# Performance work log

Hardware: AMD Instinct MI355X
Metric: run time of the kernel (lower is better)

The kernel has to match this reference:

```python
import jax, jax.numpy as jnp
import numpy as np

EPS = 1e-5

def layer_norm(x, gamma, beta):
    m = jnp.mean(x, axis=-1, keepdims=True)
    v = jnp.var(x, axis=-1, keepdims=True)
    return (x - m) / jnp.sqrt(v + EPS) * gamma + beta


def setup_inputs() -> dict:
    key = jax.random.key(0)
    ks = jax.random.split(key, 10)
    B, N, D = 2, 2048, 1024
    H, Dh = 16, 64
    C, CD = 256, 512
    inner = H * Dh  # 1024
    J = C + 1 + N  # 2305 = context + null + self

    x = jax.random.normal(ks[0], (B, N, D), dtype=jnp.float32)
    context = jax.random.normal(ks[1], (B, C, CD), dtype=jnp.float32)
    mask = jax.random.uniform(ks[2], (B, C + N)) < 0.9  # bool, mostly True
    attn_bias = jax.random.normal(ks[3], (H, N, J), dtype=jnp.float32) * 0.02

    norm_gamma = jnp.ones((D,), dtype=jnp.float32)
    null_kv = jax.random.normal(ks[4], (2, Dh), dtype=jnp.float32)
    Wq = jax.random.normal(ks[5], (D, inner), dtype=jnp.float32) * (D ** -0.5)
    Wkv = jax.random.normal(ks[6], (D, 2 * Dh), dtype=jnp.float32) * (D ** -0.5)
    ctx_ln_w = jnp.ones((CD,), dtype=jnp.float32)
    ctx_ln_b = jnp.zeros((CD,), dtype=jnp.float32)
    Wctx = jax.random.normal(ks[7], (CD, 2 * Dh), dtype=jnp.float32) * (CD ** -0.5)
    bctx = jnp.zeros((2 * Dh,), dtype=jnp.float32)
    Wout = jax.random.normal(ks[8], (inner, D), dtype=jnp.float32) * (inner ** -0.5)
    out_gamma = jnp.ones((D,), dtype=jnp.float32)

    return {"x": x, "context": context, "mask": mask, "attn_bias": attn_bias,
            "norm_gamma": norm_gamma, "null_kv": null_kv, "Wq": Wq, "Wkv": Wkv,
            "ctx_ln_w": ctx_ln_w, "ctx_ln_b": ctx_ln_b, "Wctx": Wctx, "bctx": bctx,
            "Wout": Wout, "out_gamma": out_gamma}


def reference(x, context, mask, attn_bias, norm_gamma, null_kv, Wq, Wkv,
              ctx_ln_w, ctx_ln_b, Wctx, bctx, Wout, out_gamma):
    B, N, D = x.shape
    Dh = null_kv.shape[-1]
    H = Wq.shape[-1] // Dh
    scale = Dh ** -0.5

    xn = layer_norm(x, norm_gamma, 0.0)
    q = (xn @ Wq).reshape(B, N, H, Dh).transpose(0, 2, 1, 3) * scale  # b h n d
    k, v = jnp.split(xn @ Wkv, 2, axis=-1)  # b n d each (multi-query: shared across heads)

    # prepend learned null kv token
    nk = jnp.broadcast_to(null_kv[0], (B, 1, Dh))
    nv = jnp.broadcast_to(null_kv[1], (B, 1, Dh))
    k = jnp.concatenate([nk, k], axis=1)
    v = jnp.concatenate([nv, v], axis=1)

    # prepend projected context tokens
    cn = layer_norm(context, ctx_ln_w, ctx_ln_b)
    ck, cv = jnp.split(cn @ Wctx + bctx, 2, axis=-1)
    k = jnp.concatenate([ck, k], axis=1)  # b j d, j = C + 1 + N
    v = jnp.concatenate([cv, v], axis=1)

    sim = jnp.einsum('bhid,bjd->bhij', q, k) + attn_bias
    # pad mask with True for the null token (left), then broadcast over h, i
    m = jnp.pad(mask, ((0, 0), (1, 0)), constant_values=True)[:, None, None, :]
    max_neg = -jnp.finfo(sim.dtype).max
    sim = jnp.where(m, sim, max_neg)

    attn = jax.nn.softmax(sim.astype(jnp.float32), axis=-1)
    out = jnp.einsum('bhij,bjd->bhid', attn, v)  # b h n d
    out = out.transpose(0, 2, 1, 3).reshape(B, N, H * Dh)
    return layer_norm(out @ Wout, out_gamma, 0.0)
```

## Files before the change

### kernel.cpp

```cpp
#include <hip/hip_runtime.h>

constexpr int B  = 2;
constexpr int N  = 2048;
constexpr int H  = 16;
constexpr int C  = 256;
constexpr int J  = C + 1 + N;
constexpr int Jp = 2368;
constexpr int NT = Jp / 64;
constexpr float EPS = 1e-5f;
constexpr float LOG2E = 1.4426950408889634f;

typedef __bf16 bf16x8 __attribute__((ext_vector_type(8)));
typedef float  f32x4  __attribute__((ext_vector_type(4)));
typedef unsigned int uint4v __attribute__((ext_vector_type(4)));
typedef __attribute__((address_space(3))) unsigned int lds_u32;
typedef const __attribute__((address_space(1))) unsigned int glb_u32;

__device__ inline void load_lds16(const void* g, void* l) {
    __builtin_amdgcn_global_load_lds((glb_u32*)g, (lds_u32*)l, 16, 0, 0);
}
__device__ inline unsigned short f2bf(float f) {
    unsigned int u = __builtin_bit_cast(unsigned int, f);
    u += 0x7fffu + ((u >> 16) & 1u);
    return (unsigned short)(u >> 16);
}
__device__ inline unsigned int packbf2(float a, float b) {
    union { __bf16 h[2]; unsigned int u; } cv;
    cv.h[0] = (__bf16)a;
    cv.h[1] = (__bf16)b;
    return cv.u;
}
__device__ inline float fexp2(float x) {
    float r;
    asm("v_exp_f32 %0, %1" : "=v"(r) : "v"(x));
    return r;
}
__device__ inline f32x4 mfma16(bf16x8 a, bf16x8 b, f32x4 c) {
    return __builtin_amdgcn_mfma_f32_16x16x32_bf16(a, b, c, 0, 0, 0);
}
__device__ inline f32x4 loadu4(const float* p) {
    f32x4 r;
    __builtin_memcpy(&r, p, 16);
    return r;
}

__global__ void mask_prep(const void* __restrict__ mraw, float* __restrict__ maskf) {
    __shared__ int bad_int, bad_f32;
    const int t = threadIdx.x;
    if (t == 0) { bad_int = 0; bad_f32 = 0; }
    __syncthreads();
    const unsigned int* w = (const unsigned int*)mraw;
    int li = 0, lf = 0;
    for (int i = t; i < 1152; i += 256) {
        unsigned int v = w[i];
        if (v > 1u) li = 1;
        if (v != 0u && v != 0x3F800000u) lf = 1;
    }
    if (li) atomicOr(&bad_int, 1);
    if (lf) atomicOr(&bad_f32, 1);
    __syncthreads();
    const int mode = (!bad_int) ? 0 : ((!bad_f32) ? 1 : 2);
    const unsigned char* bytes = (const unsigned char*)mraw;
    for (int i = t; i < 2 * Jp; i += 256) {
        const int b2 = i / Jp, jp = i - b2 * Jp;
        float v;
        if (jp == 0) v = 0.f;
        else if (jp >= J) v = -1e30f;
        else {
            const int idx = b2 * (C + N) + jp - 1;
            const int keep = (mode == 2) ? (bytes[idx] != 0) : (w[idx] != 0u);
            v = keep ? 0.f : -1e30f;
        }
        maskf[i] = v;
    }
}

__global__ void zero_pads(unsigned short* __restrict__ Kb, unsigned short* __restrict__ Vt) {
    const int t = threadIdx.x;
    for (int i = t; i < 2 * 63 * 64; i += 256) {
        const int b2 = i / (63 * 64);
        const int rr = (i / 64) % 63;
        const int d  = i % 64;
        Kb[(size_t)(b2 * Jp + J + rr) * 64 + d] = 0;
    }
    for (int i = t; i < 2 * 64 * 63; i += 256) {
        const int b2 = i / (64 * 63);
        const int d  = (i / 63) % 64;
        const int cc = i % 63;
        Vt[(size_t)(b2 * 64 + d) * Jp + J + cc] = 0;
    }
}

template <int BF16OUT>
__global__ void __launch_bounds__(256) ln1024(const float* __restrict__ x,
                                              const float* __restrict__ gamma,
                                              void* __restrict__ outp) {
    const int row = blockIdx.x;
    const int t = threadIdx.x;
    const float* xr = x + (size_t)row * 1024;
    float4 v = ((const float4*)xr)[t];
    float s  = v.x + v.y + v.z + v.w;
    float ss = v.x * v.x + v.y * v.y + v.z * v.z + v.w * v.w;
    #pragma unroll
    for (int o = 1; o < 64; o <<= 1) {
        s  += __shfl_xor(s, o);
        ss += __shfl_xor(ss, o);
    }
    __shared__ float red[8];
    const int w = t >> 6;
    if ((t & 63) == 0) { red[w * 2] = s; red[w * 2 + 1] = ss; }
    __syncthreads();
    s  = red[0] + red[2] + red[4] + red[6];
    ss = red[1] + red[3] + red[5] + red[7];
    const float mean = s * (1.0f / 1024.0f);
    const float var  = ss * (1.0f / 1024.0f) - mean * mean;
    const float rstd = rsqrtf(var + EPS);
    const float4 g = ((const float4*)gamma)[t];
    float o0 = (v.x - mean) * rstd * g.x;
    float o1 = (v.y - mean) * rstd * g.y;
    float o2 = (v.z - mean) * rstd * g.z;
    float o3 = (v.w - mean) * rstd * g.w;
    if (BF16OUT) {
        ushort4 u;
        u.x = f2bf(o0); u.y = f2bf(o1); u.z = f2bf(o2); u.w = f2bf(o3);
        *(ushort4*)((unsigned short*)outp + (size_t)row * 1024 + t * 4) = u;
    } else {
        *(float4*)((float*)outp + (size_t)row * 1024 + t * 4) = make_float4(o0, o1, o2, o3);
    }
}

__global__ void __launch_bounds__(256) transpose_w(const float* __restrict__ W,
                                                   unsigned short* __restrict__ WT,
                                                   int K, int Nn, float scale) {
    __shared__ float lds[64][68];
    const int k0 = blockIdx.x * 64, n0 = blockIdx.y * 64;
    const int t = threadIdx.x;
    const int kk = t >> 4, nn = (t & 15) * 4;
    #pragma unroll
    for (int r = 0; r < 4; r++) {
        const float4 v = *(const float4*)(W + (size_t)(k0 + kk + r * 16) * Nn + n0 + nn);
        lds[kk + r * 16][nn + 0] = v.x;
        lds[kk + r * 16][nn + 1] = v.y;
        lds[kk + r * 16][nn + 2] = v.z;
        lds[kk + r * 16][nn + 3] = v.w;
    }
    __syncthreads();
    const int nr = t >> 2, kc = (t & 3) * 16;
    #pragma unroll
    for (int u4 = 0; u4 < 4; u4++) {
        ushort4 u;
        u.x = f2bf(lds[kc + u4 * 4 + 0][nr] * scale);
        u.y = f2bf(lds[kc + u4 * 4 + 1][nr] * scale);
        u.z = f2bf(lds[kc + u4 * 4 + 2][nr] * scale);
        u.w = f2bf(lds[kc + u4 * 4 + 3][nr] * scale);
        *(ushort4*)(WT + (size_t)(n0 + nr) * K + k0 + kc + u4 * 4) = u;
    }
}

__global__ void __launch_bounds__(128) ctx_proj(const float* __restrict__ ctx,
                                                const float* __restrict__ lw,
                                                const float* __restrict__ lb,
                                                const float* __restrict__ Wc,
                                                const float* __restrict__ bc,
                                                unsigned short* __restrict__ Kb,
                                                unsigned short* __restrict__ Vt) {
    const int row = blockIdx.x;
    const int b2 = row >> 8, ci = row & 255;
    const int t = threadIdx.x;
    __shared__ float cn[512];
    __shared__ float red[4];
    const float* xr = ctx + (size_t)row * 512;
    float4 v = ((const float4*)xr)[t];
    float s  = v.x + v.y + v.z + v.w;
    float ss = v.x * v.x + v.y * v.y + v.z * v.z + v.w * v.w;
    #pragma unroll
    for (int o = 1; o < 64; o <<= 1) {
        s  += __shfl_xor(s, o);
        ss += __shfl_xor(ss, o);
    }
    const int w = t >> 6;
    if ((t & 63) == 0) { red[w * 2] = s; red[w * 2 + 1] = ss; }
    __syncthreads();
    s  = red[0] + red[2];
    ss = red[1] + red[3];
    const float mean = s * (1.0f / 512.0f);
    const float var  = ss * (1.0f / 512.0f) - mean * mean;
    const float rstd = rsqrtf(var + EPS);
    const float4 g  = ((const float4*)lw)[t];
    const float4 be = ((const float4*)lb)[t];
    float4 c4;
    c4.x = (v.x - mean) * rstd * g.x + be.x;
    c4.y = (v.y - mean) * rstd * g.y + be.y;
    c4.z = (v.z - mean) * rstd * g.z + be.z;
    c4.w = (v.w - mean) * rstd * g.w + be.w;
    *(float4*)&cn[t * 4] = c4;
    __syncthreads();
    float acc = bc[t];
    #pragma unroll 8
    for (int d = 0; d < 512; d++) acc = fmaf(cn[d], Wc[d * 128 + t], acc);
    const unsigned short bv = f2bf(acc);
    if (t < 64) Kb[(size_t)(b2 * Jp + ci) * 64 + t] = bv;
    else        Vt[(size_t)(b2 * 64 + (t - 64)) * Jp + ci] = bv;
}

__global__ void null_fill(const float* __restrict__ nkv,
                          unsigned short* __restrict__ Kb, unsigned short* __restrict__ Vt) {
    const int b2 = blockIdx.x;
    const int t = threadIdx.x;
    Kb[(size_t)(b2 * Jp + 256) * 64 + t] = f2bf(nkv[t]);
    Vt[(size_t)(b2 * 64 + t) * Jp + 256] = f2bf(nkv[64 + t]);
}

template <int MODE>
__global__ void __launch_bounds__(256, 2) gemm_bf16(
        const unsigned short* __restrict__ A, const unsigned short* __restrict__ BT,
        float* __restrict__ Cf, unsigned short* __restrict__ Cb,
        unsigned short* __restrict__ Kb, unsigned short* __restrict__ Vt,
        int M, int Nn, int K) {
    __shared__ __align__(16) unsigned char smem[65536];
    const int t = threadIdx.x;
    const int w = t >> 6, lane = t & 63;
    const int g = lane >> 4, ln15 = lane & 15;
    const int wm = w >> 1, wn = w & 1;
    const int row0 = blockIdx.x * 128, col0 = blockIdx.y * 128;
    const int nk = K >> 6;
    const int ls = lane >> 3;
    const int swz = (lane & 7) ^ ls;

    f32x4 acc[4][4];
    #pragma unroll
    for (int i = 0; i < 4; i++)
        #pragma unroll
        for (int jj = 0; jj < 4; jj++)
            acc[i][jj] = (f32x4){0.f, 0.f, 0.f, 0.f};

    auto stage = [&](int kt, int cur) {
        if (w < 2) {
            const unsigned short* src = A + (size_t)(row0 + w * 64 + ls) * K + kt * 64 + swz * 8;
            unsigned char* dst = smem + cur * 16384 + w * 8192;
            #pragma unroll
            for (int i = 0; i < 8; i++)
                load_lds16(src + (size_t)i * 8 * K, dst + i * 1024);
        } else {
            const unsigned short* src = BT + (size_t)(col0 + (w - 2) * 64 + ls) * K + kt * 64 + swz * 8;
            unsigned char* dst = smem + 32768 + cur * 16384 + (w - 2) * 8192;
            #pragma unroll
            for (int i = 0; i < 8; i++)
                load_lds16(src + (size_t)i * 8 * K, dst + i * 1024);
        }
    };

    stage(0, 0);
    __syncthreads();
    for (int kt = 0; kt < nk; kt++) {
        const int cur = kt & 1;
        if (kt + 1 < nk) stage(kt + 1, cur ^ 1);
        const unsigned char* As = smem + cur * 16384;
        const unsigned char* Bs = smem + 32768 + cur * 16384;
        #pragma unroll
        for (int ks = 0; ks < 2; ks++) {
            bf16x8 af[4], bf[4];
            #pragma unroll
            for (int mq = 0; mq < 4; mq++)
                af[mq] = *(const bf16x8*)(As + (wm * 64 + mq * 16 + ln15) * 128 +
                                          ((ks * 64 + g * 16) ^ ((ln15 & 7) << 4)));
            #pragma unroll
            for (int nq = 0; nq < 4; nq++)
                bf[nq] = *(const bf16x8*)(Bs + (wn * 64 + nq * 16 + ln15) * 128 +
                                          ((ks * 64 + g * 16) ^ ((ln15 & 7) << 4)));
            #pragma unroll
            for (int mq = 0; mq < 4; mq++)
                #pragma unroll
                for (int nq = 0; nq < 4; nq++)
                    acc[mq][nq] = mfma16(af[mq], bf[nq], acc[mq][nq]);
        }
        __syncthreads();
    }

    #pragma unroll
    for (int mq = 0; mq < 4; mq++) {
        #pragma unroll
        for (int nq = 0; nq < 4; nq++) {
            #pragma unroll
            for (int r = 0; r < 4; r++) {
                const int gr = row0 + wm * 64 + mq * 16 + g * 4 + r;
                const int gc = col0 + wn * 64 + nq * 16 + ln15;
                if (MODE == 0) {
                    Cf[(size_t)gr * Nn + gc] = acc[mq][nq][r];
                } else if (MODE == 1) {
                    Cb[(size_t)gr * Nn + gc] = f2bf(acc[mq][nq][r]);
                } else {
                    const int b2 = gr >> 11, tok = gr & 2047;
                    const unsigned short v = f2bf(acc[mq][nq][r]);
                    if (gc < 64) Kb[(size_t)(b2 * Jp + 257 + tok) * 64 + gc] = v;
                    else         Vt[(size_t)(b2 * 64 + gc - 64) * Jp + 257 + tok] = v;
                }
            }
        }
    }
}

__global__ void __launch_bounds__(512, 2) attn_v9(
        const unsigned short* __restrict__ qb, const unsigned short* __restrict__ Kb,
        const unsigned short* __restrict__ Vt, const float* __restrict__ bias,
        const float* __restrict__ maskf, unsigned short* __restrict__ aout) {
    __shared__ __align__(16) unsigned char smem[135168];
    const int t = threadIdx.x;
    const int w = t >> 6, lane = t & 63;
    const int g = lane >> 4, ln15 = lane & 15;
    const int i0 = blockIdx.x * 128, h = blockIdx.y;
    const int b2 = w & 1, wq = w >> 1;
    const int ls = lane >> 3;
    const int swz = (lane & 7) ^ ls;

    auto stage = [&](int jt, int cur) {
        const int j0 = jt * 64;
        const int half = w & 1;
        if (w < 4) {
            const int kb = w >> 1;
            const unsigned short* src = Kb + (size_t)(kb * Jp + j0 + half * 32 + ls) * 64 + swz * 8;
            unsigned char* dst = smem + cur * 32768 + kb * 8192 + half * 4096;
            #pragma unroll
            for (int i = 0; i < 4; i++)
                load_lds16(src + (size_t)i * 8 * 64, dst + i * 1024);
        } else {
            const int vb = (w - 4) >> 1;
            const unsigned short* src = Vt + (size_t)(vb * 64 + half * 32 + ls) * Jp + j0 + swz * 8;
            unsigned char* dst = smem + cur * 32768 + 16384 + vb * 8192 + half * 4096;
            #pragma unroll
            for (int i = 0; i < 4; i++)
                load_lds16(src + (size_t)i * 8 * Jp, dst + i * 1024);
        }
    };

    const int bq  = t >> 2;
    const int bs0 = (t & 3) * 16;
    const float* biasQrow = bias + ((size_t)h * N + i0 + bq) * J;
    auto bias_issue = [&](int jt, f32x4& r0, f32x4& r1, f32x4& r2, f32x4& r3) {
        const int j0 = jt * 64;
        if (j0 + 64 <= J) {
            r0 = loadu4(biasQrow + j0 + bs0 + 0);
            r1 = loadu4(biasQrow + j0 + bs0 + 4);
            r2 = loadu4(biasQrow + j0 + bs0 + 8);
            r3 = loadu4(biasQrow + j0 + bs0 + 12);
        } else {
            #pragma unroll
            for (int c = 0; c < 4; c++) {
                const int ja = j0 + bs0 + c;
                r0[c] = (ja      < J) ? biasQrow[ja]      : 0.f;
                r1[c] = (ja + 4  < J) ? biasQrow[ja + 4]  : 0.f;
                r2[c] = (ja + 8  < J) ? biasQrow[ja + 8]  : 0.f;
                r3[c] = (ja + 12 < J) ? biasQrow[ja + 12] : 0.f;
            }
        }
    };
    auto bias_write = [&](int cur, const f32x4& r0, const f32x4& r1,
                          const f32x4& r2, const f32x4& r3) {
        float* basep = (float*)(smem + 65536 + cur * 34816) + bq * 68 + bs0;
        *(f32x4*)(basep + 0)  = r0;
        *(f32x4*)(basep + 4)  = r1;
        *(f32x4*)(basep + 8)  = r2;
        *(f32x4*)(basep + 12) = r3;
    };

    bf16x8 qf[2][2];
    #pragma unroll
    for (int qq = 0; qq < 2; qq++)
        #pragma unroll
        for (int ks = 0; ks < 2; ks++)
            qf[qq][ks] = *(const bf16x8*)(qb +
                (size_t)(b2 * N + i0 + wq * 32 + qq * 16 + ln15) * 1024 +
                h * 64 + ks * 32 + g * 8);

    float mrun[2] = {-1e30f, -1e30f};
    float lrun[2] = {0.f, 0.f};
    f32x4 outA[2][4];
    #pragma unroll
    for (int qq = 0; qq < 2; qq++)
        #pragma unroll
        for (int nq = 0; nq < 4; nq++)
            outA[qq][nq] = (f32x4){0.f, 0.f, 0.f, 0.f};

    const int srclA = ln15 + (((2 * g + 0) & 3) << 4);
    const int srclB = ln15 + (((2 * g + 1) & 3) << 4);

    auto compute = [&](int jt, int cur) {
        const int j0 = jt * 64;
        const unsigned char* Kl = smem + cur * 32768 + b2 * 8192;
        const unsigned char* Vl = smem + cur * 32768 + 16384 + b2 * 8192;
        const float* bbase = (const float*)(smem + 65536 + cur * 34816);

        f32x4 mk[4];
        #pragma unroll
        for (int jqm = 0; jqm < 4; jqm++)
            mk[jqm] = *(const f32x4*)(maskf + b2 * Jp + j0 + jqm * 16 + g * 4);

        f32x4 S[2][4];
        #pragma unroll
        for (int qq = 0; qq < 2; qq++)
            #pragma unroll
            for (int jqm = 0; jqm < 4; jqm++)
                S[qq][jqm] = (f32x4){0.f, 0.f, 0.f, 0.f};
        #pragma unroll
        for (int ks = 0; ks < 2; ks++) {
            bf16x8 ka[4];
            #pragma unroll
            for (int jqm = 0; jqm < 4; jqm++)
                ka[jqm] = *(const bf16x8*)(Kl + (jqm * 16 + ln15) * 128 +
                                           ((ks * 64 + g * 16) ^ ((ln15 & 7) << 4)));
            __builtin_amdgcn_s_setprio(1);
            #pragma unroll
            for (int jqm = 0; jqm < 4; jqm++) {
                S[0][jqm] = mfma16(ka[jqm], qf[0][ks], S[0][jqm]);
                S[1][jqm] = mfma16(ka[jqm], qf[1][ks], S[1][jqm]);
            }
            __builtin_amdgcn_s_setprio(0);
        }

        unsigned int Wp[2][4][2];
        #pragma unroll
        for (int qq = 0; qq < 2; qq++) {
            const float* bb = bbase + (wq * 32 + qq * 16 + ln15) * 68;
            float sv[4][4];
            #pragma unroll
            for (int jqm = 0; jqm < 4; jqm++) {
                const f32x4 br = *(const f32x4*)(bb + jqm * 16 + g * 4);
                #pragma unroll
                for (int r = 0; r < 4; r++)
                    sv[jqm][r] = fmaf(br[r], LOG2E, S[qq][jqm][r]) + mk[jqm][r];
            }

            float tmj[4];
            #pragma unroll
            for (int jqm = 0; jqm < 4; jqm++)
                tmj[jqm] = fmaxf(fmaxf(sv[jqm][0], sv[jqm][1]), fmaxf(sv[jqm][2], sv[jqm][3]));
            float tm = fmaxf(fmaxf(tmj[0], tmj[1]), fmaxf(tmj[2], tmj[3]));
            tm = fmaxf(tm, __shfl_xor(tm, 16));
            tm = fmaxf(tm, __shfl_xor(tm, 32));

            if (!__all(tm <= mrun[qq])) {
                const float mnew = fmaxf(mrun[qq], tm);
                const float cor = fexp2(mrun[qq] - mnew);
                mrun[qq] = mnew;
                float corr[4];
                #pragma unroll
                for (int r = 0; r < 4; r++) corr[r] = __shfl(cor, g * 4 + r, 64);
                #pragma unroll
                for (int nq = 0; nq < 4; nq++)
                    #pragma unroll
                    for (int r = 0; r < 4; r++)
                        outA[qq][nq][r] *= corr[r];
                lrun[qq] *= cor;
            }
            const float mcur = mrun[qq];

            float p[4][4];
            #pragma unroll
            for (int jqm = 0; jqm < 4; jqm++)
                #pragma unroll
                for (int r = 0; r < 4; r++)
                    p[jqm][r] = fexp2(sv[jqm][r] - mcur);
            float tsj[4];
            #pragma unroll
            for (int jqm = 0; jqm < 4; jqm++)
                tsj[jqm] = (p[jqm][0] + p[jqm][1]) + (p[jqm][2] + p[jqm][3]);
            float ts = (tsj[0] + tsj[1]) + (tsj[2] + tsj[3]);
            ts += __shfl_xor(ts, 16);
            ts += __shfl_xor(ts, 32);
            lrun[qq] += ts;

            #pragma unroll
            for (int jqm = 0; jqm < 4; jqm++) {
                Wp[qq][jqm][0] = packbf2(p[jqm][0], p[jqm][1]);
                Wp[qq][jqm][1] = packbf2(p[jqm][2], p[jqm][3]);
            }
        }

        #pragma unroll
        for (int ks = 0; ks < 2; ks++) {
            bf16x8 pa[2];
            #pragma unroll
            for (int qq = 0; qq < 2; qq++) {
                uint4v wd;
                #pragma unroll
                for (int widx = 0; widx < 4; widx++) {
                    const int srcl = (widx >> 1) ? srclB : srclA;
                    const int t0 = __shfl((int)Wp[qq][ks * 2 + 0][widx & 1], srcl, 64);
                    const int t1 = __shfl((int)Wp[qq][ks * 2 + 1][widx & 1], srcl, 64);
                    wd[widx] = (unsigned int)((g >> 1) ? t1 : t0);
                }
                pa[qq] = __builtin_bit_cast(bf16x8, wd);
            }
            bf16x8 vf[4];
            #pragma unroll
            for (int nq = 0; nq < 4; nq++)
                vf[nq] = *(const bf16x8*)(Vl + (nq * 16 + ln15) * 128 +
                                          ((ks * 64 + g * 16) ^ ((ln15 & 7) << 4)));
            __builtin_amdgcn_s_setprio(1);
            #pragma unroll
            for (int nq = 0; nq < 4; nq++) {
                outA[0][nq] = mfma16(pa[0], vf[nq], outA[0][nq]);
                outA[1][nq] = mfma16(pa[1], vf[nq], outA[1][nq]);
            }
            __builtin_amdgcn_s_setprio(0);
        }
    };

    f32x4 bR0, bR1, bR2, bR3;
    bias_issue(0, bR0, bR1, bR2, bR3);
    stage(0, 0);
    bias_write(0, bR0, bR1, bR2, bR3);
    __syncthreads();
    for (int jt = 0; jt < NT; jt++) {
        const int cur = jt & 1;
        if (jt + 1 < NT) {
            bias_issue(jt + 1, bR0, bR1, bR2, bR3);
            stage(jt + 1, cur ^ 1);
        }
        compute(jt, cur);
        if (jt + 1 < NT) bias_write(cur ^ 1, bR0, bR1, bR2, bR3);
        __syncthreads();
    }

    #pragma unroll
    for (int qq = 0; qq < 2; qq++) {
        const float inv = 1.0f / lrun[qq];
        float invr[4];
        #pragma unroll
        for (int r = 0; r < 4; r++) invr[r] = __shfl(inv, g * 4 + r, 64);
        #pragma unroll
        for (int nq = 0; nq < 4; nq++)
            #pragma unroll
            for (int r = 0; r < 4; r++)
                aout[(size_t)(b2 * N + i0 + wq * 32 + qq * 16 + g * 4 + r) * 1024 +
                     h * 64 + nq * 16 + ln15] = f2bf(outA[qq][nq][r] * invr[r]);
    }
}

extern "C" void kernel_launch(void* const* d_in, const int* in_sizes, int n_in,
                              void* d_out, int out_size, void* d_ws, size_t ws_size,
                              hipStream_t stream) {
    const float* x         = (const float*)d_in[0];
    const float* context   = (const float*)d_in[1];
    const void*  mask      = d_in[2];
    const float* bias      = (const float*)d_in[3];
    const float* norm_g    = (const float*)d_in[4];
    const float* null_kv   = (const float*)d_in[5];
    const float* Wq        = (const float*)d_in[6];
    const float* Wkv       = (const float*)d_in[7];
    const float* ctx_ln_w  = (const float*)d_in[8];
    const float* ctx_ln_b  = (const float*)d_in[9];
    const float* Wctx      = (const float*)d_in[10];
    const float* bctx      = (const float*)d_in[11];
    const float* Wout      = (const float*)d_in[12];
    const float* out_gamma = (const float*)d_in[13];
    float* out = (float*)d_out;

    unsigned char* wsb = (unsigned char*)d_ws;
    unsigned short* xnb   = (unsigned short*)(wsb + 0);
    unsigned short* qbb   = (unsigned short*)(wsb + 8388608);
    float*          y     = (float*)(wsb + 0);
    unsigned short* aoutp = (unsigned short*)(wsb + 16777216);
    unsigned short* KbP   = (unsigned short*)(wsb + 25165824);
    unsigned short* VtP   = (unsigned short*)(wsb + 25772032);
    float*          maskf = (float*)(wsb + 26378240);
    unsigned short* WqT   = (unsigned short*)(wsb + 26397184);
    unsigned short* WkvT  = (unsigned short*)(wsb + 28494336);
    unsigned short* WoutT = (unsigned short*)(wsb + 28756480);

    mask_prep<<<1, 256, 0, stream>>>(mask, maskf);
    zero_pads<<<1, 256, 0, stream>>>(KbP, VtP);
    ln1024<1><<<B * N, 256, 0, stream>>>(x, norm_g, xnb);
    transpose_w<<<dim3(16, 16), 256, 0, stream>>>(Wq, WqT, 1024, 1024, 0.125f * LOG2E);
    transpose_w<<<dim3(16, 2), 256, 0, stream>>>(Wkv, WkvT, 1024, 128, 1.0f);
    transpose_w<<<dim3(16, 16), 256, 0, stream>>>(Wout, WoutT, 1024, 1024, 1.0f);
    ctx_proj<<<B * C, 128, 0, stream>>>(context, ctx_ln_w, ctx_ln_b, Wctx, bctx, KbP, VtP);
    null_fill<<<B, 64, 0, stream>>>(null_kv, KbP, VtP);
    gemm_bf16<1><<<dim3(32, 8), 256, 0, stream>>>(xnb, WqT, nullptr, qbb, nullptr, nullptr, 4096, 1024, 1024);
    gemm_bf16<2><<<dim3(32, 1), 256, 0, stream>>>(xnb, WkvT, nullptr, nullptr, KbP, VtP, 4096, 128, 1024);
    attn_v9<<<dim3(16, 16), 512, 0, stream>>>(qbb, KbP, VtP, bias, maskf, aoutp);
    gemm_bf16<0><<<dim3(32, 8), 256, 0, stream>>>(aoutp, WoutT, y, nullptr, nullptr, nullptr, 4096, 1024, 1024);
    ln1024<0><<<B * N, 256, 0, stream>>>(y, out_gamma, out);
}
```

Measured before the change: 273.6 us.

## Switch attention kernel to 32x32x16 MFMA tiles with per-row lane layout

Rewrites the attention inner loop so each wave computes QK^T and PV with 32x32x16 bf16 MFMAs instead of 16x16x32 ones. Each lane now owns one query row, which turns the row max and row sum reductions into a single cross-half shuffle and removes the per-row broadcast shuffles for the correction and normalisation factors. The P fragment is rebuilt with xor-32 shuffles, and the bias LDS row stride is padded from 68 to 76 floats to suit the new access pattern, which enlarges shared memory. Output stores become packed 32-bit writes. The 32x32 accumulators need more registers, which may put pressure on the two-blocks-per-CU launch bound.

```diff
diff --git a/kernel.cpp b/kernel.cpp
--- a/kernel.cpp
+++ b/kernel.cpp
@@ -12,6 +12,7 @@
 
 typedef __bf16 bf16x8 __attribute__((ext_vector_type(8)));
 typedef float  f32x4  __attribute__((ext_vector_type(4)));
+typedef float  f32x16 __attribute__((ext_vector_type(16)));
 typedef unsigned int uint4v __attribute__((ext_vector_type(4)));
 typedef __attribute__((address_space(3))) unsigned int lds_u32;
 typedef const __attribute__((address_space(1))) unsigned int glb_u32;
@@ -37,6 +38,9 @@
 }
 __device__ inline f32x4 mfma16(bf16x8 a, bf16x8 b, f32x4 c) {
     return __builtin_amdgcn_mfma_f32_16x16x32_bf16(a, b, c, 0, 0, 0);
+}
+__device__ inline f32x16 mfma32(bf16x8 a, bf16x8 b, f32x16 c) {
+    return __builtin_amdgcn_mfma_f32_32x32x16_bf16(a, b, c, 0, 0, 0);
 }
 __device__ inline f32x4 loadu4(const float* p) {
     f32x4 r;
@@ -300,18 +304,19 @@
     }
 }
 
-__global__ void __launch_bounds__(512, 2) attn_v9(
+__global__ void __launch_bounds__(512, 2) attn_v11(
         const unsigned short* __restrict__ qb, const unsigned short* __restrict__ Kb,
         const unsigned short* __restrict__ Vt, const float* __restrict__ bias,
         const float* __restrict__ maskf, unsigned short* __restrict__ aout) {
-    __shared__ __align__(16) unsigned char smem[135168];
+    __shared__ __align__(16) unsigned char smem[143360];
     const int t = threadIdx.x;
     const int w = t >> 6, lane = t & 63;
-    const int g = lane >> 4, ln15 = lane & 15;
+    const int l31 = lane & 31, hi = lane >> 5;
     const int i0 = blockIdx.x * 128, h = blockIdx.y;
     const int b2 = w & 1, wq = w >> 1;
     const int ls = lane >> 3;
     const int swz = (lane & 7) ^ ls;
+    const int rsw = (lane & 7) << 4;
 
     auto stage = [&](int jt, int cur) {
         const int j0 = jt * 64;
@@ -333,20 +338,20 @@
         }
     };
 
-    const int bq  = t >> 2;
-    const int bs0 = (t & 3) * 16;
+    const int bq = t >> 2;
+    const int bs = (t & 3) * 16;
     const float* biasQrow = bias + ((size_t)h * N + i0 + bq) * J;
     auto bias_issue = [&](int jt, f32x4& r0, f32x4& r1, f32x4& r2, f32x4& r3) {
         const int j0 = jt * 64;
         if (j0 + 64 <= J) {
-            r0 = loadu4(biasQrow + j0 + bs0 + 0);
-            r1 = loadu4(biasQrow + j0 + bs0 + 4);
-            r2 = loadu4(biasQrow + j0 + bs0 + 8);
-            r3 = loadu4(biasQrow + j0 + bs0 + 12);
+            r0 = loadu4(biasQrow + j0 + bs + 0);
+            r1 = loadu4(biasQrow + j0 + bs + 4);
+            r2 = loadu4(biasQrow + j0 + bs + 8);
+            r3 = loadu4(biasQrow + j0 + bs + 12);
         } else {
             #pragma unroll
             for (int c = 0; c < 4; c++) {
-                const int ja = j0 + bs0 + c;
+                const int ja = j0 + bs + c;
                 r0[c] = (ja      < J) ? biasQrow[ja]      : 0.f;
                 r1[c] = (ja + 4  < J) ? biasQrow[ja + 4]  : 0.f;
                 r2[c] = (ja + 8  < J) ? biasQrow[ja + 8]  : 0.f;
@@ -356,153 +361,119 @@
     };
     auto bias_write = [&](int cur, const f32x4& r0, const f32x4& r1,
                           const f32x4& r2, const f32x4& r3) {
-        float* basep = (float*)(smem + 65536 + cur * 34816) + bq * 68 + bs0;
+        float* basep = (float*)(smem + 65536 + cur * 38912) + bq * 76 + bs;
         *(f32x4*)(basep + 0)  = r0;
         *(f32x4*)(basep + 4)  = r1;
         *(f32x4*)(basep + 8)  = r2;
         *(f32x4*)(basep + 12) = r3;
     };
 
-    bf16x8 qf[2][2];
-    #pragma unroll
-    for (int qq = 0; qq < 2; qq++)
-        #pragma unroll
-        for (int ks = 0; ks < 2; ks++)
-            qf[qq][ks] = *(const bf16x8*)(qb +
-                (size_t)(b2 * N + i0 + wq * 32 + qq * 16 + ln15) * 1024 +
-                h * 64 + ks * 32 + g * 8);
-
-    float mrun[2] = {-1e30f, -1e30f};
-    float lrun[2] = {0.f, 0.f};
-    f32x4 outA[2][4];
-    #pragma unroll
-    for (int qq = 0; qq < 2; qq++)
-        #pragma unroll
-        for (int nq = 0; nq < 4; nq++)
-            outA[qq][nq] = (f32x4){0.f, 0.f, 0.f, 0.f};
-
-    const int srclA = ln15 + (((2 * g + 0) & 3) << 4);
-    const int srclB = ln15 + (((2 * g + 1) & 3) << 4);
+    bf16x8 qf[4];
+    #pragma unroll
+    for (int ks = 0; ks < 4; ks++)
+        qf[ks] = *(const bf16x8*)(qb + (size_t)(b2 * N + i0 + wq * 32 + l31) * 1024 +
+                                  h * 64 + ks * 16 + hi * 8);
+
+    float mrun = -1e30f, lrun = 0.f;
+    f32x16 outA[2];
+    outA[0] = (f32x16)0.f;
+    outA[1] = (f32x16)0.f;
 
     auto compute = [&](int jt, int cur) {
         const int j0 = jt * 64;
         const unsigned char* Kl = smem + cur * 32768 + b2 * 8192;
         const unsigned char* Vl = smem + cur * 32768 + 16384 + b2 * 8192;
-        const float* bbase = (const float*)(smem + 65536 + cur * 34816);
-
-        f32x4 mk[4];
-        #pragma unroll
-        for (int jqm = 0; jqm < 4; jqm++)
-            mk[jqm] = *(const f32x4*)(maskf + b2 * Jp + j0 + jqm * 16 + g * 4);
-
-        f32x4 S[2][4];
-        #pragma unroll
-        for (int qq = 0; qq < 2; qq++)
-            #pragma unroll
-            for (int jqm = 0; jqm < 4; jqm++)
-                S[qq][jqm] = (f32x4){0.f, 0.f, 0.f, 0.f};
-        #pragma unroll
-        for (int ks = 0; ks < 2; ks++) {
+        const float* bbL = (const float*)(smem + 65536 + cur * 38912) +
+                           (wq * 32 + l31) * 76;
+
+        f32x16 S[2];
+        S[0] = (f32x16)0.f;
+        S[1] = (f32x16)0.f;
+        #pragma unroll
+        for (int jh = 0; jh < 2; jh++) {
+            const int krow = jh * 32 + l31;
             bf16x8 ka[4];
             #pragma unroll
-            for (int jqm = 0; jqm < 4; jqm++)
-                ka[jqm] = *(const bf16x8*)(Kl + (jqm * 16 + ln15) * 128 +
-                                           ((ks * 64 + g * 16) ^ ((ln15 & 7) << 4)));
+            for (int ks = 0; ks < 4; ks++)
+                ka[ks] = *(const bf16x8*)(Kl + krow * 128 + ((ks * 32 + hi * 16) ^ rsw));
             __builtin_amdgcn_s_setprio(1);
             #pragma unroll
-            for (int jqm = 0; jqm < 4; jqm++) {
-                S[0][jqm] = mfma16(ka[jqm], qf[0][ks], S[0][jqm]);
-                S[1][jqm] = mfma16(ka[jqm], qf[1][ks], S[1][jqm]);
+            for (int ks = 0; ks < 4; ks++)
+                S[jh] = mfma32(ka[ks], qf[ks], S[jh]);
+            __builtin_amdgcn_s_setprio(0);
+        }
+
+        float sv[2][16];
+        #pragma unroll
+        for (int jh = 0; jh < 2; jh++)
+            #pragma unroll
+            for (int rg = 0; rg < 4; rg++) {
+                const f32x4 br = *(const f32x4*)(bbL + jh * 32 + rg * 8 + hi * 4);
+                const f32x4 mk = *(const f32x4*)(maskf + b2 * Jp + j0 + jh * 32 + rg * 8 + hi * 4);
+                #pragma unroll
+                for (int c = 0; c < 4; c++)
+                    sv[jh][rg * 4 + c] = fmaf(br[c], LOG2E, S[jh][rg * 4 + c]) + mk[c];
             }
-            __builtin_amdgcn_s_setprio(0);
-        }
-
-        unsigned int Wp[2][4][2];
-        #pragma unroll
-        for (int qq = 0; qq < 2; qq++) {
-            const float* bb = bbase + (wq * 32 + qq * 16 + ln15) * 68;
-            float sv[4][4];
-            #pragma unroll
-            for (int jqm = 0; jqm < 4; jqm++) {
-                const f32x4 br = *(const f32x4*)(bb + jqm * 16 + g * 4);
+
+        float tm = sv[0][0];
+        #pragma unroll
+        for (int jh = 0; jh < 2; jh++)
+            #pragma unroll
+            for (int r = 0; r < 16; r++)
+                tm = fmaxf(tm, sv[jh][r]);
+        tm = fmaxf(tm, __shfl_xor(tm, 32));
+
+        if (!__all(tm <= mrun)) {
+            const float mnew = fmaxf(mrun, tm);
+            const float cor = fexp2(mrun - mnew);
+            mrun = mnew;
+            #pragma unroll
+            for (int i = 0; i < 16; i++) { outA[0][i] *= cor; outA[1][i] *= cor; }
+            lrun *= cor;
+        }
+        const float mcur = mrun;
+
+        float p[2][16];
+        float ts = 0.f;
+        #pragma unroll
+        for (int jh = 0; jh < 2; jh++)
+            #pragma unroll
+            for (int r = 0; r < 16; r++) {
+                p[jh][r] = fexp2(sv[jh][r] - mcur);
+                ts += p[jh][r];
+            }
+        ts += __shfl_xor(ts, 32);
+        lrun += ts;
+
+        #pragma unroll
+        for (int jh = 0; jh < 2; jh++) {
+            #pragma unroll
+            for (int m = 0; m < 2; m++) {
+                const unsigned int a0 = packbf2(p[jh][m * 8 + 0], p[jh][m * 8 + 1]);
+                const unsigned int a1 = packbf2(p[jh][m * 8 + 2], p[jh][m * 8 + 3]);
+                const unsigned int b0 = packbf2(p[jh][m * 8 + 4], p[jh][m * 8 + 5]);
+                const unsigned int b1 = packbf2(p[jh][m * 8 + 6], p[jh][m * 8 + 7]);
+                const unsigned int xa0 = (unsigned int)__shfl_xor((int)a0, 32);
+                const unsigned int xa1 = (unsigned int)__shfl_xor((int)a1, 32);
+                const unsigned int xb0 = (unsigned int)__shfl_xor((int)b0, 32);
+                const unsigned int xb1 = (unsigned int)__shfl_xor((int)b1, 32);
+                uint4v wd;
+                wd[0] = hi ? xb0 : a0;
+                wd[1] = hi ? xb1 : a1;
+                wd[2] = hi ? b0 : xa0;
+                wd[3] = hi ? b1 : xa1;
+                const bf16x8 pfrag = __builtin_bit_cast(bf16x8, wd);
+                bf16x8 va[2];
                 #pragma unroll
-                for (int r = 0; r < 4; r++)
-                    sv[jqm][r] = fmaf(br[r], LOG2E, S[qq][jqm][r]) + mk[jqm][r];
+                for (int dblk = 0; dblk < 2; dblk++)
+                    va[dblk] = *(const bf16x8*)(Vl + (dblk * 32 + l31) * 128 +
+                               ((jh * 64 + m * 32 + hi * 16) ^ rsw));
+                __builtin_amdgcn_s_setprio(1);
+                #pragma unroll
+                for (int dblk = 0; dblk < 2; dblk++)
+                    outA[dblk] = mfma32(va[dblk], pfrag, outA[dblk]);
+                __builtin_amdgcn_s_setprio(0);
             }
-
-            float tmj[4];
-            #pragma unroll
-            for (int jqm = 0; jqm < 4; jqm++)
-                tmj[jqm] = fmaxf(fmaxf(sv[jqm][0], sv[jqm][1]), fmaxf(sv[jqm][2], sv[jqm][3]));
-            float tm = fmaxf(fmaxf(tmj[0], tmj[1]), fmaxf(tmj[2], tmj[3]));
-            tm = fmaxf(tm, __shfl_xor(tm, 16));
-            tm = fmaxf(tm, __shfl_xor(tm, 32));
-
-            if (!__all(tm <= mrun[qq])) {
-                const float mnew = fmaxf(mrun[qq], tm);
-                const float cor = fexp2(mrun[qq] - mnew);
-                mrun[qq] = mnew;
-                float corr[4];
-                #pragma unroll
-                for (int r = 0; r < 4; r++) corr[r] = __shfl(cor, g * 4 + r, 64);
-                #pragma unroll
-                for (int nq = 0; nq < 4; nq++)
-                    #pragma unroll
-                    for (int r = 0; r < 4; r++)
-                        outA[qq][nq][r] *= corr[r];
-                lrun[qq] *= cor;
-            }
-            const float mcur = mrun[qq];
-
-            float p[4][4];
-            #pragma unroll
-            for (int jqm = 0; jqm < 4; jqm++)
-                #pragma unroll
-                for (int r = 0; r < 4; r++)
-                    p[jqm][r] = fexp2(sv[jqm][r] - mcur);
-            float tsj[4];
-            #pragma unroll
-            for (int jqm = 0; jqm < 4; jqm++)
-                tsj[jqm] = (p[jqm][0] + p[jqm][1]) + (p[jqm][2] + p[jqm][3]);
-            float ts = (tsj[0] + tsj[1]) + (tsj[2] + tsj[3]);
-            ts += __shfl_xor(ts, 16);
-            ts += __shfl_xor(ts, 32);
-            lrun[qq] += ts;
-
-            #pragma unroll
-            for (int jqm = 0; jqm < 4; jqm++) {
-                Wp[qq][jqm][0] = packbf2(p[jqm][0], p[jqm][1]);
-                Wp[qq][jqm][1] = packbf2(p[jqm][2], p[jqm][3]);
-            }
-        }
-
-        #pragma unroll
-        for (int ks = 0; ks < 2; ks++) {
-            bf16x8 pa[2];
-            #pragma unroll
-            for (int qq = 0; qq < 2; qq++) {
-                uint4v wd;
-                #pragma unroll
-                for (int widx = 0; widx < 4; widx++) {
-                    const int srcl = (widx >> 1) ? srclB : srclA;
-                    const int t0 = __shfl((int)Wp[qq][ks * 2 + 0][widx & 1], srcl, 64);
-                    const int t1 = __shfl((int)Wp[qq][ks * 2 + 1][widx & 1], srcl, 64);
-                    wd[widx] = (unsigned int)((g >> 1) ? t1 : t0);
-                }
-                pa[qq] = __builtin_bit_cast(bf16x8, wd);
-            }
-            bf16x8 vf[4];
-            #pragma unroll
-            for (int nq = 0; nq < 4; nq++)
-                vf[nq] = *(const bf16x8*)(Vl + (nq * 16 + ln15) * 128 +
-                                          ((ks * 64 + g * 16) ^ ((ln15 & 7) << 4)));
-            __builtin_amdgcn_s_setprio(1);
-            #pragma unroll
-            for (int nq = 0; nq < 4; nq++) {
-                outA[0][nq] = mfma16(pa[0], vf[nq], outA[0][nq]);
-                outA[1][nq] = mfma16(pa[1], vf[nq], outA[1][nq]);
-            }
-            __builtin_amdgcn_s_setprio(0);
         }
     };
 
@@ -522,19 +493,18 @@
         __syncthreads();
     }
 
-    #pragma unroll
-    for (int qq = 0; qq < 2; qq++) {
-        const float inv = 1.0f / lrun[qq];
-        float invr[4];
-        #pragma unroll
-        for (int r = 0; r < 4; r++) invr[r] = __shfl(inv, g * 4 + r, 64);
-        #pragma unroll
-        for (int nq = 0; nq < 4; nq++)
-            #pragma unroll
-            for (int r = 0; r < 4; r++)
-                aout[(size_t)(b2 * N + i0 + wq * 32 + qq * 16 + g * 4 + r) * 1024 +
-                     h * 64 + nq * 16 + ln15] = f2bf(outA[qq][nq][r] * invr[r]);
-    }
+    const float inv = 1.0f / lrun;
+    unsigned short* orow = aout + (size_t)(b2 * N + i0 + wq * 32 + l31) * 1024 + h * 64;
+    #pragma unroll
+    for (int dblk = 0; dblk < 2; dblk++)
+        #pragma unroll
+        for (int rg = 0; rg < 4; rg++)
+            #pragma unroll
+            for (int c2 = 0; c2 < 2; c2++) {
+                const int r = rg * 4 + c2 * 2;
+                const unsigned int u = packbf2(outA[dblk][r] * inv, outA[dblk][r + 1] * inv);
+                *(unsigned int*)(orow + dblk * 32 + rg * 8 + hi * 4 + c2 * 2) = u;
+            }
 }
 
 extern "C" void kernel_launch(void* const* d_in, const int* in_sizes, int n_in,
@@ -578,7 +548,7 @@
     null_fill<<<B, 64, 0, stream>>>(null_kv, KbP, VtP);
     gemm_bf16<1><<<dim3(32, 8), 256, 0, stream>>>(xnb, WqT, nullptr, qbb, nullptr, nullptr, 4096, 1024, 1024);
     gemm_bf16<2><<<dim3(32, 1), 256, 0, stream>>>(xnb, WkvT, nullptr, nullptr, KbP, VtP, 4096, 128, 1024);
-    attn_v9<<<dim3(16, 16), 512, 0, stream>>>(qbb, KbP, VtP, bias, maskf, aoutp);
+    attn_v11<<<dim3(16, 16), 512, 0, stream>>>(qbb, KbP, VtP, bias, maskf, aoutp);
     gemm_bf16<0><<<dim3(32, 8), 256, 0, stream>>>(aoutp, WoutT, y, nullptr, nullptr, nullptr, 4096, 1024, 1024);
     ln1024<0><<<B * N, 256, 0, stream>>>(y, out_gamma, out);
 }
```

Measured after the change: 254.0 us. -7.2%, faster.
